# Performance work log

Measured on AMD Instinct MI355X. Metric: run time of the kernel, lower is better.

## Reference

```python
import jax, jax.numpy as jnp
import numpy as np

TWO_PI = 2.0 * np.pi


def _grid_sample(w, g):
    """Bilinear sample. w: [M,C,H,W]; g: [M,2,H,W] coords in [-1,1] (x,y),
    align_corners=True, border-clamped."""
    H, W = w.shape[-2], w.shape[-1]
    x = (g[:, 0] + 1.0) * 0.5 * (W - 1)  # [M,H,W]
    y = (g[:, 1] + 1.0) * 0.5 * (H - 1)
    x0 = jnp.floor(x)
    y0 = jnp.floor(y)
    fx = x - x0
    fy = y - y0
    x0i = jnp.clip(x0.astype(jnp.int32), 0, W - 1)
    x1i = jnp.clip(x0i + 1, 0, W - 1)
    y0i = jnp.clip(y0.astype(jnp.int32), 0, H - 1)
    y1i = jnp.clip(y0i + 1, 0, H - 1)

    def samp(wm, yi, xi):
        return wm[:, yi, xi]  # [C,H,W]

    v00 = jax.vmap(samp)(w, y0i, x0i)
    v01 = jax.vmap(samp)(w, y0i, x1i)
    v10 = jax.vmap(samp)(w, y1i, x0i)
    v11 = jax.vmap(samp)(w, y1i, x1i)
    fx = fx[:, None]  # broadcast over channel dim
    fy = fy[:, None]
    return (1 - fy) * ((1 - fx) * v00 + fx * v01) + fy * ((1 - fx) * v10 + fx * v11)


def _forward(in_H, out_H, weight, grid_H, grid_Rn, mask):
    No, Ni = out_H.shape[0], in_H.shape[0]
    N = grid_H.shape[0]
    Gk, Cout, Cin, kh, kw = weight.shape

    # inverse_H: angles negate; left_apply_to_H: angles add (pairwise)
    out_inv = -out_H  # [No,1]
    theta = (out_inv[:, None, 0] + in_H[None, :, 0]).reshape(-1)  # [No*Ni]

    # interpolate_H: periodic linear interp over uniform angle grid
    step = TWO_PI / N
    pos = jnp.mod(theta, TWO_PI) / step
    i0 = jnp.floor(pos).astype(jnp.int32) % N
    i1 = (i0 + 1) % N
    frac = (pos - jnp.floor(pos))[:, None]
    wflat = weight.reshape(Gk, -1)  # [Gk, Cout*Cin*kh*kw]
    w = (1.0 - frac) * wflat[i0] + frac * wflat[i1]  # [No*Ni, C]
    w = w.reshape(No * Ni, Cin * Cout, kh, kw)

    # left_apply_to_Rn: rotate spatial grid by out_H^{-1}
    ang = out_inv[:, 0]
    c, s = jnp.cos(ang), jnp.sin(ang)
    gx = c[:, None, None] * grid_Rn[0] - s[:, None, None] * grid_Rn[1]
    gy = s[:, None, None] * grid_Rn[0] + c[:, None, None] * grid_Rn[1]
    grids = jnp.stack([gx, gy], axis=1)  # [No,2,kh,kw]
    grids = jnp.repeat(grids, Ni, axis=0)  # repeat_interleave -> [No*Ni,2,kh,kw]

    # interpolate_Rn: bilinear grid sample
    w = _grid_sample(w, grids)  # [No*Ni, Cin*Cout, kh, kw]
    w = w.reshape(No, Ni, Cin, Cout, kh, kw)
    # .transpose(0,3).transpose(1,3) -> [Cout, No, Cin, Ni, kh, kw]
    w = jnp.transpose(w, (3, 0, 2, 1, 4, 5))
    return mask * w


def setup_inputs() -> dict:
    key = jax.random.key(0)
    k1, k2, k3 = jax.random.split(key, 3)
    N, Cout, Cin, ks = 8, 128, 128, 5
    in_H = jax.random.uniform(k1, (N, 1), dtype=jnp.float32) * TWO_PI
    out_H = jax.random.uniform(k2, (N, 1), dtype=jnp.float32) * TWO_PI
    fan_in = Cin * ks * ks
    weight = jax.random.normal(k3, (N, Cout, Cin, ks, ks), dtype=jnp.float32) / np.sqrt(fan_in)
    grid_H = (jnp.arange(N) * (TWO_PI / N)).astype(jnp.float32)
    lin = jnp.linspace(-1.0, 1.0, ks)
    X, Y = jnp.meshgrid(lin, lin, indexing='xy')
    grid_Rn = jnp.stack([X, Y]).astype(jnp.float32)  # [2, ks, ks]
    mask = (X ** 2 + Y ** 2 <= 1.0 + 1e-6).astype(jnp.float32)  # circular mask
    return dict(in_H=in_H, out_H=out_H, weight=weight, grid_H=grid_H,
                grid_Rn=grid_Rn, mask=mask)


def reference(in_H, out_H, weight, grid_H, grid_Rn, mask):
    return _forward(in_H, out_H, weight, grid_H, grid_Rn, mask)
```

## Files before the change

kernel.cpp:

```cpp
#include <hip/hip_runtime.h>
#include <math.h>


#define TWO_PI_F 6.28318530717958647692f

__global__ __launch_bounds__(256) void rotconv_weight_kernel(
    const float* __restrict__ in_H,
    const float* __restrict__ out_H,
    const float* __restrict__ weight,
    const float* __restrict__ grid_Rn,
    const float* __restrict__ mask,
    float* __restrict__ out)
{
    __shared__ __align__(16) float s_tile[256 * 25];

    const int t  = threadIdx.x;
    const int bx = blockIdx.x;
    const int vt = bx & 7;
    const int ut = (bx >> 3) & 7;
    const int i  = (bx >> 6) & 7;
    const int o  = bx >> 9;
    const int u0 = ut * 16;
    const int v0 = vt * 16;

    const float ang = -out_H[o];

    const float theta = in_H[i] + ang;
    float m = fmodf(theta, TWO_PI_F);
    if (m < 0.0f) m += TWO_PI_F;
    const float pos  = m * (8.0f / TWO_PI_F);
    const float pf   = floorf(pos);
    const float frac = pos - pf;
    const int g0 = ((int)pf) & 7;
    const int g1 = (g0 + 1) & 7;
    const float om = 1.0f - frac;

    const int grp = t / 25;
    const int k   = t - grp * 25;
    int rb0, rb1;
    float w00, w01, w10, w11;
    {
        float sthe, cthe;
        sincosf(ang, &sthe, &cthe);
        const float X = grid_Rn[k];
        const float Y = grid_Rn[25 + k];
        const float gx = cthe * X - sthe * Y;
        const float gy = sthe * X + cthe * Y;
        const float x = (gx + 1.0f) * 2.0f;
        const float y = (gy + 1.0f) * 2.0f;
        const float x0f = floorf(x);
        const float y0f = floorf(y);
        const float fx = x - x0f;
        const float fy = y - y0f;
        int x0 = (int)x0f; x0 = x0 < 0 ? 0 : (x0 > 4 ? 4 : x0);
        int y0 = (int)y0f; y0 = y0 < 0 ? 0 : (y0 > 4 ? 4 : y0);
        const int y1 = y0 + 1 > 4 ? 4 : y0 + 1;
        const float mk = mask[k];
        float wa = mk * (1.0f - fy) * (1.0f - fx);
        float wb = mk * (1.0f - fy) * fx;
        float wc = mk * fy * (1.0f - fx);
        float wd = mk * fy * fx;
        int xb = x0;
        if (x0 == 4) { xb = 3; wb += wa; wa = 0.0f; wd += wc; wc = 0.0f; }
        rb0 = y0 * 5 + xb;
        rb1 = y1 * 5 + xb;
        w00 = wa; w01 = wb; w10 = wc; w11 = wd;
    }

    const size_t b0 = ((size_t)(g0 * 128 + u0) * 128 + v0) * 25;
    const size_t b1 = ((size_t)(g1 * 128 + u0) * 128 + v0) * 25;
    for (int f4 = t; f4 < 1600; f4 += 256) {
        const int chunk = f4 / 100;
        const int off4  = f4 - chunk * 100;
        const size_t a  = (size_t)chunk * 3200 + (size_t)off4 * 4;
        const float4 a0 = *reinterpret_cast<const float4*>(weight + b0 + a);
        const float4 a1 = *reinterpret_cast<const float4*>(weight + b1 + a);
        float4 bl;
        bl.x = om * a0.x + frac * a1.x;
        bl.y = om * a0.y + frac * a1.y;
        bl.z = om * a0.z + frac * a1.z;
        bl.w = om * a0.w + frac * a1.w;
        *reinterpret_cast<float4*>(s_tile + (size_t)f4 * 4) = bl;
    }

    __syncthreads();

    const size_t obase = ((((size_t)v0 * 8 + o) * 128 + u0) * 8 + i) * 25 + k;
    if (grp < 10) {
#pragma unroll 4
        for (int run = grp; run < 256; run += 10) {
            const int uu = run >> 4;
            const int vv = run & 15;
            const float* tp = s_tile + run * 25;
            const float v00 = tp[rb0];
            const float v01 = tp[rb0 + 1];
            const float v10 = tp[rb1];
            const float v11 = tp[rb1 + 1];
            out[obase + (size_t)vv * 204800 + (size_t)uu * 200] =
                w00 * v00 + w01 * v01 + w10 * v10 + w11 * v11;
        }
    }
}

extern "C" void kernel_launch(void* const* d_in, const int* in_sizes, int n_in,
                              void* d_out, int out_size, void* d_ws, size_t ws_size,
                              hipStream_t stream) {
    const float* in_H    = (const float*)d_in[0];
    const float* out_H   = (const float*)d_in[1];
    const float* weight  = (const float*)d_in[2];
    const float* grid_Rn = (const float*)d_in[4];
    const float* mask    = (const float*)d_in[5];
    float* out = (float*)d_out;

    rotconv_weight_kernel<<<dim3(4096), dim3(256), 0, stream>>>(
        in_H, out_H, weight, grid_Rn, mask, out);
}
```

Before: 145.1 us.

## Stage all 8 angle groups per block and fold angle interpolation into coefficients

Each block now covers a 16x2 (u,v) tile for all eight input angles instead of a 16x16 tile for one angle. It loads the weight slices for all eight groups into shared memory once, so weight data is no longer reread once per input angle. The angular interpolation weights are folded into the bilinear coefficients, giving eight shared-memory reads per output. Threads map to (i,k), so each thread row writes 200 contiguous floats, which should coalesce stores better. In exchange, loads become narrower float2 accesses, 56 of 256 threads sit idle during compute, and the compute path does more shared-memory reads per output.

```diff
diff --git a/kernel.cpp b/kernel.cpp
--- a/kernel.cpp
+++ b/kernel.cpp
@@ -3,6 +3,7 @@
 
 
 #define TWO_PI_F 6.28318530717958647692f
+#define G_STRIDE 808
 
 __global__ __launch_bounds__(256) void rotconv_weight_kernel(
     const float* __restrict__ in_H,
@@ -12,16 +13,30 @@
     const float* __restrict__ mask,
     float* __restrict__ out)
 {
-    __shared__ __align__(16) float s_tile[256 * 25];
+    __shared__ __align__(16) float s_w[8 * G_STRIDE];
 
     const int t  = threadIdx.x;
     const int bx = blockIdx.x;
-    const int vt = bx & 7;
-    const int ut = (bx >> 3) & 7;
-    const int i  = (bx >> 6) & 7;
+    const int vt = bx & 63;
+    const int ut = (bx >> 6) & 7;
     const int o  = bx >> 9;
     const int u0 = ut * 16;
-    const int v0 = vt * 16;
+    const int v0 = vt * 2;
+
+    for (int j = t; j < 3200; j += 256) {
+        const int chunk = j / 25;
+        const int off   = j - chunk * 25;
+        const int g = chunk >> 4;
+        const int u = chunk & 15;
+        const float2 w2 = *reinterpret_cast<const float2*>(
+            weight + ((size_t)((g * 128 + u0 + u) * 128) + v0) * 25 + (size_t)off * 2);
+        *reinterpret_cast<float2*>(s_w + g * G_STRIDE + u * 50 + off * 2) = w2;
+    }
+
+    const int ii = t / 25;
+    const int k  = t - ii * 25;
+    const bool active = (t < 200);
+    const int i = ii > 7 ? 7 : ii;
 
     const float ang = -out_H[o];
 
@@ -35,69 +50,56 @@
     const int g1 = (g0 + 1) & 7;
     const float om = 1.0f - frac;
 
-    const int grp = t / 25;
-    const int k   = t - grp * 25;
-    int rb0, rb1;
-    float w00, w01, w10, w11;
-    {
-        float sthe, cthe;
-        sincosf(ang, &sthe, &cthe);
-        const float X = grid_Rn[k];
-        const float Y = grid_Rn[25 + k];
-        const float gx = cthe * X - sthe * Y;
-        const float gy = sthe * X + cthe * Y;
-        const float x = (gx + 1.0f) * 2.0f;
-        const float y = (gy + 1.0f) * 2.0f;
-        const float x0f = floorf(x);
-        const float y0f = floorf(y);
-        const float fx = x - x0f;
-        const float fy = y - y0f;
-        int x0 = (int)x0f; x0 = x0 < 0 ? 0 : (x0 > 4 ? 4 : x0);
-        int y0 = (int)y0f; y0 = y0 < 0 ? 0 : (y0 > 4 ? 4 : y0);
-        const int y1 = y0 + 1 > 4 ? 4 : y0 + 1;
-        const float mk = mask[k];
-        float wa = mk * (1.0f - fy) * (1.0f - fx);
-        float wb = mk * (1.0f - fy) * fx;
-        float wc = mk * fy * (1.0f - fx);
-        float wd = mk * fy * fx;
-        int xb = x0;
-        if (x0 == 4) { xb = 3; wb += wa; wa = 0.0f; wd += wc; wc = 0.0f; }
-        rb0 = y0 * 5 + xb;
-        rb1 = y1 * 5 + xb;
-        w00 = wa; w01 = wb; w10 = wc; w11 = wd;
-    }
-
-    const size_t b0 = ((size_t)(g0 * 128 + u0) * 128 + v0) * 25;
-    const size_t b1 = ((size_t)(g1 * 128 + u0) * 128 + v0) * 25;
-    for (int f4 = t; f4 < 1600; f4 += 256) {
-        const int chunk = f4 / 100;
-        const int off4  = f4 - chunk * 100;
-        const size_t a  = (size_t)chunk * 3200 + (size_t)off4 * 4;
-        const float4 a0 = *reinterpret_cast<const float4*>(weight + b0 + a);
-        const float4 a1 = *reinterpret_cast<const float4*>(weight + b1 + a);
-        float4 bl;
-        bl.x = om * a0.x + frac * a1.x;
-        bl.y = om * a0.y + frac * a1.y;
-        bl.z = om * a0.z + frac * a1.z;
-        bl.w = om * a0.w + frac * a1.w;
-        *reinterpret_cast<float4*>(s_tile + (size_t)f4 * 4) = bl;
-    }
+    float sthe, cthe;
+    sincosf(ang, &sthe, &cthe);
+    const float X = grid_Rn[k];
+    const float Y = grid_Rn[25 + k];
+    const float gx = cthe * X - sthe * Y;
+    const float gy = sthe * X + cthe * Y;
+    const float x = (gx + 1.0f) * 2.0f;
+    const float y = (gy + 1.0f) * 2.0f;
+    const float x0f = floorf(x);
+    const float y0f = floorf(y);
+    const float fx = x - x0f;
+    const float fy = y - y0f;
+    int x0 = (int)x0f; x0 = x0 < 0 ? 0 : (x0 > 4 ? 4 : x0);
+    int y0 = (int)y0f; y0 = y0 < 0 ? 0 : (y0 > 4 ? 4 : y0);
+    const int y1 = y0 + 1 > 4 ? 4 : y0 + 1;
+    const float mk = mask[k];
+    float wa = mk * (1.0f - fy) * (1.0f - fx);
+    float wb = mk * (1.0f - fy) * fx;
+    float wc = mk * fy * (1.0f - fx);
+    float wd = mk * fy * fx;
+    int xb = x0;
+    if (x0 == 4) { xb = 3; wb += wa; wa = 0.0f; wd += wc; wc = 0.0f; }
+    const int rb0 = y0 * 5 + xb;
+    const int rb1 = y1 * 5 + xb;
+    const float a00 = om * wa,  a01 = om * wb,  a10 = om * wc,  a11 = om * wd;
+    const float b00 = frac * wa, b01 = frac * wb, b10 = frac * wc, b11 = frac * wd;
 
     __syncthreads();
 
-    const size_t obase = ((((size_t)v0 * 8 + o) * 128 + u0) * 8 + i) * 25 + k;
-    if (grp < 10) {
-#pragma unroll 4
-        for (int run = grp; run < 256; run += 10) {
-            const int uu = run >> 4;
-            const int vv = run & 15;
-            const float* tp = s_tile + run * 25;
-            const float v00 = tp[rb0];
-            const float v01 = tp[rb0 + 1];
-            const float v10 = tp[rb1];
-            const float v11 = tp[rb1 + 1];
-            out[obase + (size_t)vv * 204800 + (size_t)uu * 200] =
-                w00 * v00 + w01 * v01 + w10 * v10 + w11 * v11;
+    if (!active) return;
+
+    const float* tg0 = s_w + g0 * G_STRIDE;
+    const float* tg1 = s_w + g1 * G_STRIDE;
+    const size_t ob0 = (((size_t)v0 * 8 + o) * 128 + u0) * 200 + t;
+    const size_t ob1 = ((((size_t)v0 + 1) * 8 + o) * 128 + u0) * 200 + t;
+
+#pragma unroll
+    for (int uu = 0; uu < 16; ++uu) {
+#pragma unroll
+        for (int vv = 0; vv < 2; ++vv) {
+            const int run = uu * 2 + vv;
+            const float* p0 = tg0 + run * 25;
+            const float* p1 = tg1 + run * 25;
+            const float v00 = p0[rb0], v01 = p0[rb0 + 1];
+            const float v10 = p0[rb1], v11 = p0[rb1 + 1];
+            const float w00 = p1[rb0], w01 = p1[rb0 + 1];
+            const float w10 = p1[rb1], w11 = p1[rb1 + 1];
+            const float val = a00 * v00 + a01 * v01 + a10 * v10 + a11 * v11
+                            + b00 * w00 + b01 * w01 + b10 * w10 + b11 * w11;
+            out[(vv ? ob1 : ob0) + (size_t)uu * 200] = val;
         }
     }
 }
```

After: 149.4 us. +3.0%, slower.
